# Performance work log

Hardware: AMD Instinct MI355X
Metric: run time of the kernel (lower is better)

## Reference

```python
import jax, jax.numpy as jnp
import numpy as np


def setup_inputs() -> dict:
    key = jax.random.key(0)
    k1, k2, k3, k4 = jax.random.split(key, 4)
    B, IN_DIM, OUT_DIM = 2048, 4096, 4096
    inputs = jax.random.normal(k1, (B, IN_DIM), dtype=jnp.float32)
    # integer weight code: each element of the implicit (in_dim,out_dim) weight
    # matrix is an index into the per-row `mean` vector of length in_dim
    indices = jax.random.randint(k2, (IN_DIM, OUT_DIM), 0, IN_DIM, dtype=jnp.int32)
    mean = jax.random.normal(k3, (IN_DIM,), dtype=jnp.float32)
    bias = jax.random.normal(k4, (OUT_DIM,), dtype=jnp.float32)
    return {"inputs": inputs, "indices": indices, "mean": mean, "bias": bias}


def reference(inputs, indices, mean, bias):
    # 'unsort' op: decode weight W[i,j] = mean[indices[i,j]], then x @ W
    W = mean[indices]                      # (in_dim, out_dim) gather-decode
    out = jnp.einsum("bi,io->bo", inputs, W)  # (batch, out_dim)
    return out + bias                      # channels_last bias add
```

## Files before the change

### kernel.cpp

```cpp
#include <hip/hip_runtime.h>
#include <hip/hip_bf16.h>


#define M_DIM 2048
#define K_DIM 4096
#define N_DIM 4096

#define BM 128
#define BN 256
#define BK 64
#define NT (K_DIM / BK)
#define LDSA_BYTES (BM * BK * 2)
#define LDSB_BYTES (BN * BK * 2)
#define LDS_TILE   (LDSA_BYTES + LDSB_BYTES)

typedef __attribute__((ext_vector_type(8))) short short8v;
typedef __attribute__((ext_vector_type(4))) float f32x4;

__device__ __forceinline__ unsigned short f2bf(float x) {
    unsigned u = __builtin_bit_cast(unsigned, x);
    u += 0x7fffu + ((u >> 16) & 1u);
    return (unsigned short)(u >> 16);
}

__device__ __forceinline__ void gload_lds16(const void* g, void* l) {
    __builtin_amdgcn_global_load_lds(
        (const __attribute__((address_space(1))) void*)(uintptr_t)g,
        (__attribute__((address_space(3))) void*)(uintptr_t)l, 16, 0, 0);
}

__global__ void convert_a_kernel(const float* __restrict__ A,
                                 unsigned short* __restrict__ Abf) {
    int i = blockIdx.x * blockDim.x + threadIdx.x;
    const float4 v = ((const float4*)A)[i];
    ushort4 o;
    o.x = f2bf(v.x); o.y = f2bf(v.y); o.z = f2bf(v.z); o.w = f2bf(v.w);
    ((ushort4*)Abf)[i] = o;
}

__global__ void decode_transpose_kernel(const int* __restrict__ idx,
                                        const float* __restrict__ mean,
                                        unsigned short* __restrict__ Wt) {
    __shared__ float smean[K_DIM];
    __shared__ unsigned short tile[64][65];
    const int t = threadIdx.x;
    for (int i = t; i < K_DIM; i += 256) smean[i] = mean[i];
    __syncthreads();

    const int k0 = blockIdx.y * 64;
    const int n0 = blockIdx.x * 64;
    const int rb = t >> 4;
    const int cb = (t & 15) * 4;

    #pragma unroll
    for (int i = 0; i < 4; ++i) {
        const int r = rb + i * 16;
        const int4 v = *(const int4*)&idx[(size_t)(k0 + r) * N_DIM + n0 + cb];
        tile[cb + 0][r] = f2bf(smean[v.x]);
        tile[cb + 1][r] = f2bf(smean[v.y]);
        tile[cb + 2][r] = f2bf(smean[v.z]);
        tile[cb + 3][r] = f2bf(smean[v.w]);
    }
    __syncthreads();

    #pragma unroll
    for (int i = 0; i < 4; ++i) {
        const int r = rb + i * 16;
        ushort4 o;
        o.x = tile[r][cb + 0];
        o.y = tile[r][cb + 1];
        o.z = tile[r][cb + 2];
        o.w = tile[r][cb + 3];
        *(ushort4*)&Wt[(size_t)(n0 + r) * K_DIM + k0 + cb] = o;
    }
}


#define VM6  asm volatile("s_waitcnt vmcnt(6)" ::: "memory")
#define VM0  asm volatile("s_waitcnt vmcnt(0)" ::: "memory")

#define STG6(buf, t) do {                           \
    const int ko_ = (t) * BK;                       \
    gload_lds16(sA0 + ko_, (buf) + lA0);            \
    gload_lds16(sA1 + ko_, (buf) + lA1);            \
    gload_lds16(sB0 + ko_, (buf) + lB0);            \
    gload_lds16(sB1 + ko_, (buf) + lB1);            \
    gload_lds16(sB2 + ko_, (buf) + lB2);            \
    gload_lds16(sB3 + ko_, (buf) + lB3);            \
} while (0)

#define READ8(aS, bS, buf, so) do {                 \
    aS[0] = *(const short8v*)((buf) + rA0 + (so));  \
    aS[1] = *(const short8v*)((buf) + rA1 + (so));  \
    aS[2] = *(const short8v*)((buf) + rA2 + (so));  \
    aS[3] = *(const short8v*)((buf) + rA3 + (so));  \
    bS[0] = *(const short8v*)((buf) + rB0 + (so));  \
    bS[1] = *(const short8v*)((buf) + rB1 + (so));  \
    bS[2] = *(const short8v*)((buf) + rB2 + (so));  \
    bS[3] = *(const short8v*)((buf) + rB3 + (so));  \
} while (0)

#define MM1(aS, bS, i, j) \
    acc[i][j] = __builtin_amdgcn_mfma_f32_16x16x32_bf16(aS[i], bS[j], acc[i][j], 0, 0, 0)

#define MM16(aS, bS) do {                                            \
    MM1(aS,bS,0,0); MM1(aS,bS,0,1); MM1(aS,bS,0,2); MM1(aS,bS,0,3);  \
    MM1(aS,bS,1,0); MM1(aS,bS,1,1); MM1(aS,bS,1,2); MM1(aS,bS,1,3);  \
    MM1(aS,bS,2,0); MM1(aS,bS,2,1); MM1(aS,bS,2,2); MM1(aS,bS,2,3);  \
    MM1(aS,bS,3,0); MM1(aS,bS,3,1); MM1(aS,bS,3,2); MM1(aS,bS,3,3);  \
} while (0)

#define ITER(cbuf, sbuf, tstage) do {               \
    READ8(aE, bE, cbuf, 0);                         \
    READ8(aO, bO, cbuf, so1);                       \
    STG6(sbuf, tstage);                             \
    __builtin_amdgcn_s_setprio(1);                  \
    MM16(aE, bE);                                   \
    MM16(aO, bO);                                   \
    __builtin_amdgcn_s_setprio(0);                  \
    VM6;                                            \
    __builtin_amdgcn_s_barrier();                   \
} while (0)

#define ITER_NOSTG(cbuf, WAITC) do {                \
    READ8(aE, bE, cbuf, 0);                         \
    READ8(aO, bO, cbuf, so1);                       \
    __builtin_amdgcn_s_setprio(1);                  \
    MM16(aE, bE);                                   \
    MM16(aO, bO);                                   \
    __builtin_amdgcn_s_setprio(0);                  \
    WAITC;                                          \
    __builtin_amdgcn_s_barrier();                   \
} while (0)

__global__ __launch_bounds__(512, 2) void gemm_kernel(
        const unsigned short* __restrict__ Abf,
        const unsigned short* __restrict__ Wt,
        const float* __restrict__ bias,
        float* __restrict__ C) {
    __shared__ __align__(128) char lds[3 * LDS_TILE];

    const int tid  = threadIdx.x;
    const int lane = tid & 63;
    const int w    = tid >> 6;
    const int wm   = w >> 2;
    const int wn   = w & 3;
    const int lr   = lane & 15;
    const int kq   = lane >> 4;

    const int bid = blockIdx.x;
    const int wg  = (bid & 7) * 32 + (bid >> 3);
    const int m0  = (wg >> 4) * BM;
    const int n0  = (wg & 15) * BN;

    const int pA0 = tid,        pA1 = 512 + tid;
    const int pB0 = tid,        pB1 = 512 + tid;
    const int pB2 = 1024 + tid, pB3 = 1536 + tid;
    const unsigned short* sA0 = Abf + (size_t)(m0 + (pA0 >> 3)) * K_DIM + 8 * ((pA0 & 7) ^ ((pA0 >> 3) & 7));
    const unsigned short* sA1 = Abf + (size_t)(m0 + (pA1 >> 3)) * K_DIM + 8 * ((pA1 & 7) ^ ((pA1 >> 3) & 7));
    const unsigned short* sB0 = Wt  + (size_t)(n0 + (pB0 >> 3)) * K_DIM + 8 * ((pB0 & 7) ^ ((pB0 >> 3) & 7));
    const unsigned short* sB1 = Wt  + (size_t)(n0 + (pB1 >> 3)) * K_DIM + 8 * ((pB1 & 7) ^ ((pB1 >> 3) & 7));
    const unsigned short* sB2 = Wt  + (size_t)(n0 + (pB2 >> 3)) * K_DIM + 8 * ((pB2 & 7) ^ ((pB2 >> 3) & 7));
    const unsigned short* sB3 = Wt  + (size_t)(n0 + (pB3 >> 3)) * K_DIM + 8 * ((pB3 & 7) ^ ((pB3 >> 3) & 7));
    const int lA0 = pA0 * 16,              lA1 = pA1 * 16;
    const int lB0 = LDSA_BYTES + pB0 * 16, lB1 = LDSA_BYTES + pB1 * 16;
    const int lB2 = LDSA_BYTES + pB2 * 16, lB3 = LDSA_BYTES + pB3 * 16;

    const int c0  = kq ^ (lr & 7);
    const int sc  = c0 * 16;
    const int so1 = ((c0 ^ 4) - c0) * 16;
    const int rA0 = (wm * 64 +  0 + lr) * 128 + sc;
    const int rA1 = (wm * 64 + 16 + lr) * 128 + sc;
    const int rA2 = (wm * 64 + 32 + lr) * 128 + sc;
    const int rA3 = (wm * 64 + 48 + lr) * 128 + sc;
    const int rB0 = LDSA_BYTES + (wn * 64 +  0 + lr) * 128 + sc;
    const int rB1 = LDSA_BYTES + (wn * 64 + 16 + lr) * 128 + sc;
    const int rB2 = LDSA_BYTES + (wn * 64 + 32 + lr) * 128 + sc;
    const int rB3 = LDSA_BYTES + (wn * 64 + 48 + lr) * 128 + sc;

    char* b0v = (char*)lds;
    char* b1v = (char*)lds + LDS_TILE;
    char* b2v = (char*)lds + 2 * LDS_TILE;

    f32x4 acc[4][4] = {};
    short8v aE[4], bE[4], aO[4], bO[4];

    STG6(b0v, 0);
    STG6(b1v, 1);
    VM6;
    __builtin_amdgcn_s_barrier();

    for (int tt = 0; tt < 20; ++tt) {
        const int t = tt * 3;
        ITER(b0v, b2v, t + 2);
        ITER(b1v, b0v, t + 3);
        ITER(b2v, b1v, t + 4);
    }
    ITER(b0v, b2v, 62);
    ITER(b1v, b0v, 63);
    ITER_NOSTG(b2v, VM0);
    {
        READ8(aE, bE, b0v, 0);
        READ8(aO, bO, b0v, so1);
        __builtin_amdgcn_s_setprio(1);
        MM16(aE, bE);
        MM16(aO, bO);
        __builtin_amdgcn_s_setprio(0);
    }

    #pragma unroll
    for (int j = 0; j < 4; ++j) {
        const int n = n0 + wn * 64 + j * 16 + lr;
        const float bv = bias[n];
        #pragma unroll
        for (int i = 0; i < 4; ++i) {
            const int mb = m0 + wm * 64 + i * 16 + kq * 4;
            #pragma unroll
            for (int q = 0; q < 4; ++q)
                C[(size_t)(mb + q) * N_DIM + n] = acc[i][j][q] + bv;
        }
    }
}

extern "C" void kernel_launch(void* const* d_in, const int* in_sizes, int n_in,
                              void* d_out, int out_size, void* d_ws, size_t ws_size,
                              hipStream_t stream) {
    const float* inputs  = (const float*)d_in[0];
    const int*   indices = (const int*)  d_in[1];
    const float* mean    = (const float*)d_in[2];
    const float* bias    = (const float*)d_in[3];
    float* out = (float*)d_out;

    unsigned short* Abf = (unsigned short*)d_ws;
    unsigned short* Wt  = (unsigned short*)((char*)d_ws + (size_t)M_DIM * K_DIM * 2);

    convert_a_kernel<<<(M_DIM * K_DIM / 4) / 256, 256, 0, stream>>>(inputs, Abf);
    decode_transpose_kernel<<<dim3(N_DIM / 64, K_DIM / 64), 256, 0, stream>>>(indices, mean, Wt);
    gemm_kernel<<<256, 512, 0, stream>>>(Abf, Wt, bias, out);
}
```

Baseline: 203.1 us.

## Double-buffer LDS fragments in registers to overlap reads with MFMA

Restructures the main GEMM loop so each iteration loads the next K-tile's A/B fragments from LDS into a second register set while MFMAs run on the previously loaded set. The prologue now prefetches three stages and preloads the first fragments, and the epilogue drains the remaining two tiles. This hides LDS read latency behind matrix math but doubles fragment register usage, which risks spills or register pressure under the 512-thread, 2-block launch bounds.

```diff
diff --git a/kernel.cpp b/kernel.cpp
--- a/kernel.cpp
+++ b/kernel.cpp
@@ -76,8 +76,9 @@
 }
 
 
-#define VM6  asm volatile("s_waitcnt vmcnt(6)" ::: "memory")
-#define VM0  asm volatile("s_waitcnt vmcnt(0)" ::: "memory")
+#define VM6   asm volatile("s_waitcnt vmcnt(6)" ::: "memory")
+#define VM0   asm volatile("s_waitcnt vmcnt(0)" ::: "memory")
+#define LGKM0 asm volatile("s_waitcnt lgkmcnt(0)" ::: "memory")
 
 #define STG6(buf, t) do {                           \
     const int ko_ = (t) * BK;                       \
@@ -89,48 +90,48 @@
     gload_lds16(sB3 + ko_, (buf) + lB3);            \
 } while (0)
 
-#define READ8(aS, bS, buf, so) do {                 \
-    aS[0] = *(const short8v*)((buf) + rA0 + (so));  \
-    aS[1] = *(const short8v*)((buf) + rA1 + (so));  \
-    aS[2] = *(const short8v*)((buf) + rA2 + (so));  \
-    aS[3] = *(const short8v*)((buf) + rA3 + (so));  \
-    bS[0] = *(const short8v*)((buf) + rB0 + (so));  \
-    bS[1] = *(const short8v*)((buf) + rB1 + (so));  \
-    bS[2] = *(const short8v*)((buf) + rB2 + (so));  \
-    bS[3] = *(const short8v*)((buf) + rB3 + (so));  \
-} while (0)
-
-#define MM1(aS, bS, i, j) \
-    acc[i][j] = __builtin_amdgcn_mfma_f32_16x16x32_bf16(aS[i], bS[j], acc[i][j], 0, 0, 0)
-
-#define MM16(aS, bS) do {                                            \
-    MM1(aS,bS,0,0); MM1(aS,bS,0,1); MM1(aS,bS,0,2); MM1(aS,bS,0,3);  \
-    MM1(aS,bS,1,0); MM1(aS,bS,1,1); MM1(aS,bS,1,2); MM1(aS,bS,1,3);  \
-    MM1(aS,bS,2,0); MM1(aS,bS,2,1); MM1(aS,bS,2,2); MM1(aS,bS,2,3);  \
-    MM1(aS,bS,3,0); MM1(aS,bS,3,1); MM1(aS,bS,3,2); MM1(aS,bS,3,3);  \
-} while (0)
-
-#define ITER(cbuf, sbuf, tstage) do {               \
-    READ8(aE, bE, cbuf, 0);                         \
-    READ8(aO, bO, cbuf, so1);                       \
-    STG6(sbuf, tstage);                             \
-    __builtin_amdgcn_s_setprio(1);                  \
-    MM16(aE, bE);                                   \
-    MM16(aO, bO);                                   \
-    __builtin_amdgcn_s_setprio(0);                  \
-    VM6;                                            \
-    __builtin_amdgcn_s_barrier();                   \
-} while (0)
-
-#define ITER_NOSTG(cbuf, WAITC) do {                \
-    READ8(aE, bE, cbuf, 0);                         \
-    READ8(aO, bO, cbuf, so1);                       \
-    __builtin_amdgcn_s_setprio(1);                  \
-    MM16(aE, bE);                                   \
-    MM16(aO, bO);                                   \
-    __builtin_amdgcn_s_setprio(0);                  \
-    WAITC;                                          \
-    __builtin_amdgcn_s_barrier();                   \
+#define READF(aS, bS, buf) do {                          \
+    aS[0] = *(const short8v*)((buf) + rA0);              \
+    aS[1] = *(const short8v*)((buf) + rA1);              \
+    aS[2] = *(const short8v*)((buf) + rA2);              \
+    aS[3] = *(const short8v*)((buf) + rA3);              \
+    bS[0] = *(const short8v*)((buf) + rB0);              \
+    bS[1] = *(const short8v*)((buf) + rB1);              \
+    bS[2] = *(const short8v*)((buf) + rB2);              \
+    bS[3] = *(const short8v*)((buf) + rB3);              \
+    aS[4] = *(const short8v*)((buf) + rA0 + so1);        \
+    aS[5] = *(const short8v*)((buf) + rA1 + so1);        \
+    aS[6] = *(const short8v*)((buf) + rA2 + so1);        \
+    aS[7] = *(const short8v*)((buf) + rA3 + so1);        \
+    bS[4] = *(const short8v*)((buf) + rB0 + so1);        \
+    bS[5] = *(const short8v*)((buf) + rB1 + so1);        \
+    bS[6] = *(const short8v*)((buf) + rB2 + so1);        \
+    bS[7] = *(const short8v*)((buf) + rB3 + so1);        \
+} while (0)
+
+#define MM1(aS, bS, ia, jb, i, j) \
+    acc[i][j] = __builtin_amdgcn_mfma_f32_16x16x32_bf16(aS[ia], bS[jb], acc[i][j], 0, 0, 0)
+
+#define MMALL(aS, bS) do {                                                           \
+    MM1(aS,bS,0,0,0,0); MM1(aS,bS,0,1,0,1); MM1(aS,bS,0,2,0,2); MM1(aS,bS,0,3,0,3);  \
+    MM1(aS,bS,1,0,1,0); MM1(aS,bS,1,1,1,1); MM1(aS,bS,1,2,1,2); MM1(aS,bS,1,3,1,3);  \
+    MM1(aS,bS,2,0,2,0); MM1(aS,bS,2,1,2,1); MM1(aS,bS,2,2,2,2); MM1(aS,bS,2,3,2,3);  \
+    MM1(aS,bS,3,0,3,0); MM1(aS,bS,3,1,3,1); MM1(aS,bS,3,2,3,2); MM1(aS,bS,3,3,3,3);  \
+    MM1(aS,bS,4,4,0,0); MM1(aS,bS,4,5,0,1); MM1(aS,bS,4,6,0,2); MM1(aS,bS,4,7,0,3);  \
+    MM1(aS,bS,5,4,1,0); MM1(aS,bS,5,5,1,1); MM1(aS,bS,5,6,1,2); MM1(aS,bS,5,7,1,3);  \
+    MM1(aS,bS,6,4,2,0); MM1(aS,bS,6,5,2,1); MM1(aS,bS,6,6,2,2); MM1(aS,bS,6,7,2,3);  \
+    MM1(aS,bS,7,4,3,0); MM1(aS,bS,7,5,3,1); MM1(aS,bS,7,6,3,2); MM1(aS,bS,7,7,3,3);  \
+} while (0)
+
+#define BODY(bufRd, bufSt, tstg, cA, cB, nA, nB) do {  \
+    READF(nA, nB, bufRd);                              \
+    STG6(bufSt, tstg);                                 \
+    __builtin_amdgcn_s_setprio(1);                     \
+    MMALL(cA, cB);                                     \
+    __builtin_amdgcn_s_setprio(0);                     \
+    LGKM0;                                             \
+    VM6;                                               \
+    __builtin_amdgcn_s_barrier();                      \
 } while (0)
 
 __global__ __launch_bounds__(512, 2) void gemm_kernel(
@@ -183,30 +184,39 @@
     char* b2v = (char*)lds + 2 * LDS_TILE;
 
     f32x4 acc[4][4] = {};
-    short8v aE[4], bE[4], aO[4], bO[4];
+    short8v aE[8], bE[8], aO[8], bO[8];
 
     STG6(b0v, 0);
     STG6(b1v, 1);
+    STG6(b2v, 2);
     VM6;
     __builtin_amdgcn_s_barrier();
-
-    for (int tt = 0; tt < 20; ++tt) {
-        const int t = tt * 3;
-        ITER(b0v, b2v, t + 2);
-        ITER(b1v, b0v, t + 3);
-        ITER(b2v, b1v, t + 4);
-    }
-    ITER(b0v, b2v, 62);
-    ITER(b1v, b0v, 63);
-    ITER_NOSTG(b2v, VM0);
-    {
-        READ8(aE, bE, b0v, 0);
-        READ8(aO, bO, b0v, so1);
-        __builtin_amdgcn_s_setprio(1);
-        MM16(aE, bE);
-        MM16(aO, bO);
-        __builtin_amdgcn_s_setprio(0);
-    }
+    READF(aE, bE, b0v);
+    LGKM0;
+    __builtin_amdgcn_s_barrier();
+
+    for (int tt = 0; tt < 10; ++tt) {
+        const int t = tt * 6;
+        BODY(b1v, b0v, t + 3, aE, bE, aO, bO);
+        BODY(b2v, b1v, t + 4, aO, bO, aE, bE);
+        BODY(b0v, b2v, t + 5, aE, bE, aO, bO);
+        BODY(b1v, b0v, t + 6, aO, bO, aE, bE);
+        BODY(b2v, b1v, t + 7, aE, bE, aO, bO);
+        BODY(b0v, b2v, t + 8, aO, bO, aE, bE);
+    }
+    BODY(b1v, b0v, 63, aE, bE, aO, bO);
+    READF(aE, bE, b2v);
+    __builtin_amdgcn_s_setprio(1);
+    MMALL(aO, bO);
+    __builtin_amdgcn_s_setprio(0);
+    LGKM0;
+    VM0;
+    __builtin_amdgcn_s_barrier();
+    READF(aO, bO, b0v);
+    __builtin_amdgcn_s_setprio(1);
+    MMALL(aE, bE);
+    MMALL(aO, bO);
+    __builtin_amdgcn_s_setprio(0);
 
     #pragma unroll
     for (int j = 0; j < 4; ++j) {
```

Result: slower. 208.8 us (+2.8%).
